# Kernel optimization log

Hardware: AMD Instinct MI355X
Metric: run time of the kernel (lower is better)

## Reference

```python
import jax, jax.numpy as jnp
import numpy as np

B_CAPS = 32   # number of capsule types
K = 3         # kernel size
P = 4         # pose matrix side
STRIDE = 2
ITERS = 3
PSIZE = P * P
LN_2PI = np.float32(np.log(2.0 * np.pi))


def setup_inputs() -> dict:
    key = jax.random.key(0)
    k1, k2, k3, k4, k5 = jax.random.split(key, 5)
    b, h, w = 32, 32, 32
    x = jax.random.normal(k1, (b, h, w, B_CAPS, PSIZE), jnp.float32)
    a = jax.random.uniform(k2, (b, h, w, B_CAPS, 1), jnp.float32)
    # learned params (torch: weights (1,1,1,K*K,B,P,P), beta_u/beta_a (B,1))
    weights = jax.random.normal(k3, (K * K, B_CAPS, P, P), jnp.float32)
    beta_u = 0.1 * jax.random.normal(k4, (B_CAPS, 1), jnp.float32)
    beta_a = 0.1 * jax.random.normal(k5, (B_CAPS, 1), jnp.float32)
    return {"x": x, "a": a, "weights": weights, "beta_u": beta_u, "beta_a": beta_a}


def _patch(t):
    # t: (b, h, w, B, psize) -> (b, oh, ow, K*K, B, psize)
    b, h, w = t.shape[0], t.shape[1], t.shape[2]
    starts = np.arange(0, h - K + 1, STRIDE)
    idxs = starts[:, None] + np.arange(K)[None, :]          # (oh, K) static gather indices
    oh = idxs.shape[0]
    t = t[:, idxs]                                           # (b, oh, K, w, B, ps)
    t = t[:, :, :, idxs]                                     # (b, oh, K, ow, K, B, ps)
    t = jnp.transpose(t, (0, 1, 3, 2, 4, 5, 6))              # (b, oh, ow, K, K, B, ps)
    return t.reshape(b, oh, oh, K * K, t.shape[-2], t.shape[-1]), oh


def _em_routing(v, a_in, beta_u, beta_a):
    # v: (b,h,w,Bk,C,psize)  a_in: (b,h,w,Bk,C)   Bk = K*K, C = B_CAPS
    eps = 1e-6
    lam = 1e-3
    b, h, w, Bk, C, ps = v.shape
    mu = sigma_sq = a_out = None
    for it in range(ITERS):
        if it == 0:
            r = a_in / C                                                    # (b,h,w,Bk,C)
        else:
            ln_pjh = (-(v - mu) ** 2 / (2.0 * sigma_sq)
                      - jnp.log(jnp.sqrt(sigma_sq)) - 0.5 * LN_2PI)         # (b,h,w,Bk,C,ps)
            ln_ap = ln_pjh.sum(axis=5) + jnp.log(a_out.reshape(b, h, w, 1, C))
            r = jax.nn.softmax(ln_ap, axis=4)
        r_sum = r.sum(axis=3, keepdims=True)                                # (b,h,w,1,C)
        coeff = (r / (r_sum + eps))[..., None]                              # (b,h,w,Bk,C,1)
        mu = jnp.sum(coeff * v, axis=3, keepdims=True)                      # (b,h,w,1,C,ps)
        sigma_sq = jnp.sum(coeff * (v - mu) ** 2, axis=3, keepdims=True) + eps
        cost_h = (beta_u + jnp.log(jnp.sqrt(sigma_sq))) * r_sum[..., None]  # (b,h,w,1,C,ps)
        a_out = jax.nn.sigmoid(lam * (beta_a - cost_h.sum(axis=5, keepdims=True)))
    return mu.reshape(b, h, w, C, ps), a_out.reshape(b, h, w, C, 1)


def reference(x, a, weights, beta_u, beta_a):
    b = x.shape[0]
    p_in, oh = _patch(x)                                    # (b,oh,ow,K*K,B,psize)
    a_in, _ = _patch(a)                                     # (b,oh,ow,K*K,B,1)
    p = p_in.reshape(b, oh, oh, K * K, B_CAPS, P, P)
    # voting: per-window, per-type 4x4 pose matmul
    v = jnp.einsum('bhwkcpq,kcqr->bhwkcpr', p, weights).reshape(b, oh, oh, K * K, B_CAPS, PSIZE)
    a_in = a_in.reshape(b, oh, oh, K * K, B_CAPS)
    return _em_routing(v, a_in, beta_u, beta_a)
```

## Files before the change

kernel.cpp:

```cpp
#include <hip/hip_runtime.h>
#include <math.h>

#define PP 9
#define CAPS 32
#define PS 16
#define OH 15
#define HH 32
#define WW 32
#define LN_2PI 1.8378770664093453f

typedef float f32x2 __attribute__((ext_vector_type(2)));

__device__ __forceinline__ float frcp(float x) {
    float r;
    asm("v_rcp_f32 %0, %1" : "=v"(r) : "v"(x));
    return r;
}
__device__ __forceinline__ f32x2 splat2(float x) {
    f32x2 r; r.x = x; r.y = x; return r;
}
__device__ __forceinline__ f32x2 pkfma(f32x2 a, f32x2 b, f32x2 c) {
    return __builtin_elementwise_fma(a, b, c);
}

template <int CTRL>
__device__ __forceinline__ float dppf(float x) {
    int r = __builtin_amdgcn_update_dpp(0, __builtin_bit_cast(int, x), CTRL, 0xF, 0xF, true);
    return __builtin_bit_cast(float, r);
}
__device__ __forceinline__ float row_sum16(float x) {
    x += dppf<0xB1>(x);
    x += dppf<0x4E>(x);
    x += dppf<0x124>(x);
    x += dppf<0x128>(x);
    return x;
}
__device__ __forceinline__ float row_max16(float x) {
    x = fmaxf(x, dppf<0xB1>(x));
    x = fmaxf(x, dppf<0x4E>(x));
    x = fmaxf(x, dppf<0x124>(x));
    x = fmaxf(x, dppf<0x128>(x));
    return x;
}
__device__ __forceinline__ float swz_xor16(float x) {
    return __builtin_bit_cast(float,
        __builtin_amdgcn_ds_swizzle(__builtin_bit_cast(int, x), 0x401F));
}

__global__ __launch_bounds__(64, 2) void emcaps_kernel(
    const float* __restrict__ x,
    const float* __restrict__ a,
    const float* __restrict__ wgt,
    const float* __restrict__ beta_u,
    const float* __restrict__ beta_a,
    float* __restrict__ out_mu,
    float* __restrict__ out_a)
{
    const int lane = threadIdx.x;
    const int s = lane >> 5;
    const int c = lane & 31;

    const int site = blockIdx.x * 2 + s;
    const int j = site % OH;
    const int t2 = site / OH;
    const int i = t2 % OH;
    const int b = t2 / OH;
    const int h0 = 2 * i, w0 = 2 * j;

    f32x2 v[PP][8];
    float r[PP];
    #pragma unroll
    for (int k = 0; k < PP; ++k) {
        const int hh = h0 + k / 3, ww = w0 + k % 3;
        const size_t pix = (size_t)(b * HH + hh) * WW + ww;
        const float* xb = x + pix * (CAPS * PS) + c * PS;
        *(float4*)&v[k][0] = *(const float4*)xb;
        *(float4*)&v[k][2] = *(const float4*)(xb + 4);
        *(float4*)&v[k][4] = *(const float4*)(xb + 8);
        *(float4*)&v[k][6] = *(const float4*)(xb + 12);
        r[k] = a[pix * CAPS + c] * (1.f / 32.f);
    }

    #pragma unroll
    for (int k = 0; k < PP; ++k) {
        float xt[PS];
        #pragma unroll
        for (int m = 0; m < 8; ++m) { xt[2 * m] = v[k][m].x; xt[2 * m + 1] = v[k][m].y; }
        f32x2 w2[8];
        const float* wb = wgt + k * (CAPS * PS) + c * PS;
        *(float4*)&w2[0] = *(const float4*)wb;
        *(float4*)&w2[2] = *(const float4*)(wb + 4);
        *(float4*)&w2[4] = *(const float4*)(wb + 8);
        *(float4*)&w2[6] = *(const float4*)(wb + 12);
        #pragma unroll
        for (int m = 0; m < 8; ++m) {
            f32x2 acc = splat2(0.f);
            #pragma unroll
            for (int q = 0; q < 4; ++q)
                acc = pkfma(splat2(xt[4 * (m >> 1) + q]), w2[q * 2 + (m & 1)], acc);
            v[k][m] = acc;
        }
    }

    const float bu = beta_u[c];
    const float ba = beta_a[c];
    const float eps = 1e-6f;
    const float lam = 1e-3f;

    f32x2 mu2[8], is22[8];
    float aoc = 0.f;
    float slgfull = 0.f;
    float r_sum;

    for (int it = 0; it < 3; ++it) {
        if (it > 0) {
            const float addc = __logf(aoc) - slgfull - 8.f * LN_2PI;
            float lnk[PP], red[PP];
            #pragma unroll
            for (int k = 0; k < PP; ++k) {
                f32x2 s2 = splat2(0.f);
                #pragma unroll
                for (int m = 0; m < 8; ++m) {
                    f32x2 d = v[k][m] - mu2[m];
                    s2 = pkfma(d * d, is22[m], s2);
                }
                lnk[k] = addc - (s2.x + s2.y);
            }
            #pragma unroll
            for (int k = 0; k < PP; ++k) red[k] = row_max16(lnk[k]);
            #pragma unroll
            for (int k = 0; k < PP; ++k)
                red[k] = fmaxf(red[k], swz_xor16(red[k]));
            #pragma unroll
            for (int k = 0; k < PP; ++k) lnk[k] = __expf(lnk[k] - red[k]);
            #pragma unroll
            for (int k = 0; k < PP; ++k) red[k] = row_sum16(lnk[k]);
            #pragma unroll
            for (int k = 0; k < PP; ++k)
                red[k] += swz_xor16(red[k]);
            #pragma unroll
            for (int k = 0; k < PP; ++k) r[k] = lnk[k] * frcp(red[k]);
        }

        r_sum = 0.f;
        #pragma unroll
        for (int k = 0; k < PP; ++k) r_sum += r[k];
        const float invr = frcp(r_sum + eps);
        f32x2 rr[PP];
        #pragma unroll
        for (int k = 0; k < PP; ++k) { r[k] *= invr; rr[k] = splat2(r[k]); }

        #pragma unroll
        for (int m = 0; m < 8; ++m) {
            f32x2 acc = splat2(0.f);
            #pragma unroll
            for (int k = 0; k < PP; ++k) acc = pkfma(rr[k], v[k][m], acc);
            mu2[m] = acc;
        }
        float slg = 0.f;
        #pragma unroll
        for (int m = 0; m < 8; ++m) {
            f32x2 acc = splat2(0.f);
            #pragma unroll
            for (int k = 0; k < PP; ++k) {
                f32x2 d = v[k][m] - mu2[m];
                acc = pkfma(rr[k] * d, d, acc);
            }
            f32x2 sg = acc + splat2(eps);
            is22[m].x = frcp(2.f * sg.x);
            is22[m].y = frcp(2.f * sg.y);
            slg += 0.5f * __logf(sg.x * sg.y);
        }
        slgfull = slg;
        const float ch = r_sum * (16.f * bu + slgfull);
        aoc = frcp(1.f + __expf(-lam * (ba - ch)));
    }

    float* ob = out_mu + (size_t)site * (CAPS * PS) + c * PS;
    *(float4*)(ob + 0)  = *(float4*)&mu2[0];
    *(float4*)(ob + 4)  = *(float4*)&mu2[2];
    *(float4*)(ob + 8)  = *(float4*)&mu2[4];
    *(float4*)(ob + 12) = *(float4*)&mu2[6];
    out_a[(size_t)site * CAPS + c] = aoc;
}

extern "C" void kernel_launch(void* const* d_in, const int* in_sizes, int n_in,
                              void* d_out, int out_size, void* d_ws, size_t ws_size,
                              hipStream_t stream) {
    const float* x      = (const float*)d_in[0];
    const float* a      = (const float*)d_in[1];
    const float* wgt    = (const float*)d_in[2];
    const float* beta_u = (const float*)d_in[3];
    const float* beta_a = (const float*)d_in[4];

    float* out_mu = (float*)d_out;
    float* out_a  = (float*)d_out + (size_t)32 * OH * OH * CAPS * PS;

    const int n_sites = 32 * OH * OH;
    emcaps_kernel<<<n_sites / 2, 64, 0, stream>>>(x, a, wgt, beta_u, beta_a, out_mu, out_a);
}
```

Baseline: 38.05 us.

## Store votes as packed fp16 to halve registers and raise occupancy

After: 103.3 us. 2.71x slower.

```diff
diff --git a/kernel.cpp b/kernel.cpp
--- a/kernel.cpp
+++ b/kernel.cpp
@@ -10,6 +10,7 @@
 #define LN_2PI 1.8378770664093453f
 
 typedef float f32x2 __attribute__((ext_vector_type(2)));
+typedef _Float16 f16x2 __attribute__((ext_vector_type(2)));
 
 __device__ __forceinline__ float frcp(float x) {
     float r;
@@ -21,6 +22,19 @@
 }
 __device__ __forceinline__ f32x2 pkfma(f32x2 a, f32x2 b, f32x2 c) {
     return __builtin_elementwise_fma(a, b, c);
+}
+
+__device__ __forceinline__ f16x2 pk_f16(f32x2 v) {
+    f16x2 h;
+    h.x = (_Float16)v.x;
+    h.y = (_Float16)v.y;
+    return h;
+}
+__device__ __forceinline__ f32x2 unpk(f16x2 h) {
+    f32x2 r;
+    r.x = (float)h.x;
+    r.y = (float)h.y;
+    return r;
 }
 
 template <int CTRL>
@@ -47,7 +61,7 @@
         __builtin_amdgcn_ds_swizzle(__builtin_bit_cast(int, x), 0x401F));
 }
 
-__global__ __launch_bounds__(64, 2) void emcaps_kernel(
+__global__ __launch_bounds__(64, 4) void emcaps_kernel(
     const float* __restrict__ x,
     const float* __restrict__ a,
     const float* __restrict__ wgt,
@@ -67,38 +81,37 @@
     const int b = t2 / OH;
     const int h0 = 2 * i, w0 = 2 * j;
 
-    f32x2 v[PP][8];
+    f16x2 vb[PP][8];
     float r[PP];
+
     #pragma unroll
     for (int k = 0; k < PP; ++k) {
         const int hh = h0 + k / 3, ww = w0 + k % 3;
         const size_t pix = (size_t)(b * HH + hh) * WW + ww;
         const float* xb = x + pix * (CAPS * PS) + c * PS;
-        *(float4*)&v[k][0] = *(const float4*)xb;
-        *(float4*)&v[k][2] = *(const float4*)(xb + 4);
-        *(float4*)&v[k][4] = *(const float4*)(xb + 8);
-        *(float4*)&v[k][6] = *(const float4*)(xb + 12);
+        float xt[PS];
+        *(float4*)&xt[0]  = *(const float4*)xb;
+        *(float4*)&xt[4]  = *(const float4*)(xb + 4);
+        *(float4*)&xt[8]  = *(const float4*)(xb + 8);
+        *(float4*)&xt[12] = *(const float4*)(xb + 12);
         r[k] = a[pix * CAPS + c] * (1.f / 32.f);
-    }
-
-    #pragma unroll
-    for (int k = 0; k < PP; ++k) {
-        float xt[PS];
-        #pragma unroll
-        for (int m = 0; m < 8; ++m) { xt[2 * m] = v[k][m].x; xt[2 * m + 1] = v[k][m].y; }
-        f32x2 w2[8];
+
+        float wl[PS];
         const float* wb = wgt + k * (CAPS * PS) + c * PS;
-        *(float4*)&w2[0] = *(const float4*)wb;
-        *(float4*)&w2[2] = *(const float4*)(wb + 4);
-        *(float4*)&w2[4] = *(const float4*)(wb + 8);
-        *(float4*)&w2[6] = *(const float4*)(wb + 12);
+        *(float4*)&wl[0]  = *(const float4*)wb;
+        *(float4*)&wl[4]  = *(const float4*)(wb + 4);
+        *(float4*)&wl[8]  = *(const float4*)(wb + 8);
+        *(float4*)&wl[12] = *(const float4*)(wb + 12);
+
         #pragma unroll
         for (int m = 0; m < 8; ++m) {
             f32x2 acc = splat2(0.f);
             #pragma unroll
-            for (int q = 0; q < 4; ++q)
-                acc = pkfma(splat2(xt[4 * (m >> 1) + q]), w2[q * 2 + (m & 1)], acc);
-            v[k][m] = acc;
+            for (int q = 0; q < 4; ++q) {
+                f32x2 w2; w2.x = wl[q * 4 + ((2 * m) & 3)]; w2.y = wl[q * 4 + ((2 * m + 1) & 3)];
+                acc = pkfma(splat2(xt[((2 * m) & 12) + q]), w2, acc);
+            }
+            vb[k][m] = pk_f16(acc);
         }
     }
 
@@ -112,6 +125,7 @@
     float slgfull = 0.f;
     float r_sum;
 
+    #pragma unroll 1
     for (int it = 0; it < 3; ++it) {
         if (it > 0) {
             const float addc = __logf(aoc) - slgfull - 8.f * LN_2PI;
@@ -121,7 +135,7 @@
                 f32x2 s2 = splat2(0.f);
                 #pragma unroll
                 for (int m = 0; m < 8; ++m) {
-                    f32x2 d = v[k][m] - mu2[m];
+                    f32x2 d = unpk(vb[k][m]) - mu2[m];
                     s2 = pkfma(d * d, is22[m], s2);
                 }
                 lnk[k] = addc - (s2.x + s2.y);
@@ -146,15 +160,14 @@
         #pragma unroll
         for (int k = 0; k < PP; ++k) r_sum += r[k];
         const float invr = frcp(r_sum + eps);
-        f32x2 rr[PP];
-        #pragma unroll
-        for (int k = 0; k < PP; ++k) { r[k] *= invr; rr[k] = splat2(r[k]); }
+        #pragma unroll
+        for (int k = 0; k < PP; ++k) r[k] *= invr;
 
         #pragma unroll
         for (int m = 0; m < 8; ++m) {
             f32x2 acc = splat2(0.f);
             #pragma unroll
-            for (int k = 0; k < PP; ++k) acc = pkfma(rr[k], v[k][m], acc);
+            for (int k = 0; k < PP; ++k) acc = pkfma(splat2(r[k]), unpk(vb[k][m]), acc);
             mu2[m] = acc;
         }
         float slg = 0.f;
@@ -163,8 +176,8 @@
             f32x2 acc = splat2(0.f);
             #pragma unroll
             for (int k = 0; k < PP; ++k) {
-                f32x2 d = v[k][m] - mu2[m];
-                acc = pkfma(rr[k] * d, d, acc);
+                f32x2 d = unpk(vb[k][m]) - mu2[m];
+                acc = pkfma(splat2(r[k]) * d, d, acc);
             }
             f32x2 sg = acc + splat2(eps);
             is22[m].x = frcp(2.f * sg.x);
```
